# Kernel tuning notes

Measured on AMD Instinct MI355X. Metric: run time of the kernel, lower is better.

The kernel has to match this reference:

```python
import jax, jax.numpy as jnp
import numpy as np

B, S, L, D, H, F, V = 8, 1024, 12, 768, 12, 3072, 21128
TITLE_LEN, CONTENTS_LEN = 64, 960
DH = D // H
NEG_INF = -1e9


def setup_inputs() -> dict:
    key = jax.random.key(0)
    ks = jax.random.split(key, 14)
    p = lambda k, shape: (0.02 * jax.random.normal(k, shape)).astype(jnp.float32)
    return {
        "x": jax.random.randint(ks[0], (B, S), 0, V),
        "y": jax.random.randint(ks[1], (B, CONTENTS_LEN), 0, V),
        "word_emb": p(ks[2], (V, D)),
        "pos_emb": p(ks[3], (S, D)),
        "type_emb": p(ks[4], (2, D)),
        "emb_ln_g": jnp.ones((D,), jnp.float32),
        "emb_ln_b": jnp.zeros((D,), jnp.float32),
        "Wq": p(ks[5], (L, D, D)), "bq": jnp.zeros((L, D), jnp.float32),
        "Wk": p(ks[6], (L, D, D)), "bk": jnp.zeros((L, D), jnp.float32),
        "Wv": p(ks[7], (L, D, D)), "bv": jnp.zeros((L, D), jnp.float32),
        "Wo": p(ks[8], (L, D, D)), "bo": jnp.zeros((L, D), jnp.float32),
        "ln1_g": jnp.ones((L, D), jnp.float32), "ln1_b": jnp.zeros((L, D), jnp.float32),
        "W1": p(ks[9], (L, D, F)), "b1": jnp.zeros((L, F), jnp.float32),
        "W2": p(ks[10], (L, F, D)), "b2": jnp.zeros((L, D), jnp.float32),
        "ln2_g": jnp.ones((L, D), jnp.float32), "ln2_b": jnp.zeros((L, D), jnp.float32),
        "cls_W": p(ks[11], (D, V)), "cls_b": jnp.zeros((V,), jnp.float32),
    }


def _ln(x, g, b):
    m = x.mean(-1, keepdims=True)
    v = jnp.mean((x - m) ** 2, -1, keepdims=True)
    return (x - m) * jax.lax.rsqrt(v + 1e-12) * g + b


def _forward(x, y, word_emb, pos_emb, type_emb, emb_ln_g, emb_ln_b,
             Wq, bq, Wk, bk, Wv, bv, Wo, bo, ln1_g, ln1_b,
             W1, b1, W2, b2, ln2_g, ln2_b, cls_W, cls_b):
    # prefix-LM mask: causal (tril) except fully-visible title block [S,S]
    mask = jnp.tril(jnp.ones((S, S), jnp.float32))
    mask = mask.at[:TITLE_LEN, :TITLE_LEN].set(1.0)
    bias = (1.0 - mask) * NEG_INF  # additive attention bias

    h = word_emb[x] + pos_emb[None, :, :] + type_emb[0]  # [B,S,D]
    h = _ln(h, emb_ln_g, emb_ln_b)

    scale = 1.0 / np.sqrt(DH).astype(np.float32)

    def step(h, p):
        Wq_, bq_, Wk_, bk_, Wv_, bv_, Wo_, bo_, g1, bb1, W1_, bf1, W2_, bf2, g2, bb2 = p
        q = (h @ Wq_ + bq_).reshape(B, S, H, DH)
        k = (h @ Wk_ + bk_).reshape(B, S, H, DH)
        v = (h @ Wv_ + bv_).reshape(B, S, H, DH)
        scores = jnp.einsum('bqhd,bkhd->bhqk', q, k) * scale + bias  # [B,H,S,S]
        a = jax.nn.softmax(scores, axis=-1)
        ctx = jnp.einsum('bhqk,bkhd->bqhd', a, v).reshape(B, S, D)
        h = _ln(h + ctx @ Wo_ + bo_, g1, bb1)
        ffn = jax.nn.gelu(h @ W1_ + bf1, approximate=False) @ W2_ + bf2
        h = _ln(h + ffn, g2, bb2)
        return h, None

    h, _ = jax.lax.scan(step, h, (Wq, bq, Wk, bk, Wv, bv, Wo, bo,
                                  ln1_g, ln1_b, W1, b1, W2, b2, ln2_g, ln2_b))

    logits = h[:, -CONTENTS_LEN:, :] @ cls_W + cls_b  # [B,C,V]
    logp = jax.nn.log_softmax(logits, axis=-1)
    valid = (y != -100)
    yc = jnp.where(valid, y, 0)
    nll = -jnp.take_along_axis(logp, yc[..., None], axis=-1)[..., 0]
    return jnp.sum(nll * valid) / jnp.maximum(jnp.sum(valid), 1)


def reference(x, y, word_emb, pos_emb, type_emb, emb_ln_g, emb_ln_b,
              Wq, bq, Wk, bk, Wv, bv, Wo, bo, ln1_g, ln1_b,
              W1, b1, W2, b2, ln2_g, ln2_b, cls_W, cls_b):
    return _forward(x, y, word_emb, pos_emb, type_emb, emb_ln_g, emb_ln_b,
                    Wq, bq, Wk, bk, Wv, bv, Wo, bo, ln1_g, ln1_b,
                    W1, b1, W2, b2, ln2_g, ln2_b, cls_W, cls_b)
```

## Files before the change

kernel.cpp:

```cpp
#include <hip/hip_runtime.h>

#define BB 8
#define SS 1024
#define LL 12
#define DD 768
#define HH 12
#define FF 3072
#define VV 21128
#define DH 64
#define CLEN 960
#define NROWS (BB * CLEN)
#define TOKS (BB * SS)
#define NQKV 2304
#define QKW 1536

typedef __attribute__((ext_vector_type(8))) short bh8;
typedef __attribute__((ext_vector_type(4))) float f32x4;
typedef __attribute__((ext_vector_type(4))) unsigned short us4;

__device__ __forceinline__ float bf2f(unsigned short u) {
    union { unsigned int i; float f; } c; c.i = ((unsigned int)u) << 16; return c.f;
}
__device__ __forceinline__ unsigned short f2bf(float f) {
    union { float f; unsigned int i; } c; c.f = f;
    unsigned int r = c.i + 0x7fffu + ((c.i >> 16) & 1u);
    return (unsigned short)(r >> 16);
}

#define GLOAD16(gsrc, ldst)                                                              \
    __builtin_amdgcn_global_load_lds((const __attribute__((address_space(1))) unsigned int*)(gsrc), \
                                     (__attribute__((address_space(3))) unsigned int*)(ldst), 16, 0, 0)

__device__ __forceinline__ float bsum256(float v, float* red) {
#pragma unroll
    for (int o = 32; o; o >>= 1) v += __shfl_down(v, o);
    if ((threadIdx.x & 63) == 0) red[threadIdx.x >> 6] = v;
    __syncthreads();
    float r = red[0] + red[1] + red[2] + red[3];
    __syncthreads();
    return r;
}

__global__ void transpose_f32_bf16(const float* __restrict__ in, unsigned short* __restrict__ out,
                                   int R, int C) {
    __shared__ float tile[32][33];
    int c0 = blockIdx.x << 5, r0 = blockIdx.y << 5;
    int tx = threadIdx.x, ty = threadIdx.y;
    for (int i = ty; i < 32; i += 8) {
        int r = r0 + i, c = c0 + tx;
        if (r < R && c < C) tile[i][tx] = in[(size_t)r * C + c];
    }
    __syncthreads();
    for (int i = ty; i < 32; i += 8) {
        int oc = c0 + i, orr = r0 + tx;
        if (oc < C && orr < R) out[(size_t)oc * R + orr] = f2bf(tile[tx][i]);
    }
}

__global__ void transpose_layer(const float* __restrict__ Wq, const float* __restrict__ Wk,
                                const float* __restrict__ Wv, const float* __restrict__ Wo,
                                const float* __restrict__ W1, const float* __restrict__ W2,
                                unsigned short* __restrict__ wqkvT, unsigned short* __restrict__ woT,
                                unsigned short* __restrict__ w1T, unsigned short* __restrict__ w2T) {
    __shared__ float tile[32][33];
    int t = blockIdx.x;
    const float* src;
    unsigned short* dst;
    int R, C, txt, tt;
    if (t < 1728) {
        int which = t / 576; tt = t % 576;
        src = which == 0 ? Wq : (which == 1 ? Wk : Wv);
        dst = wqkvT + (size_t)which * DD * DD; R = DD; C = DD; txt = 24;
    } else if (t < 2304) {
        tt = t - 1728; src = Wo; dst = woT; R = DD; C = DD; txt = 24;
    } else if (t < 4608) {
        tt = t - 2304; src = W1; dst = w1T; R = DD; C = FF; txt = 96;
    } else {
        tt = t - 4608; src = W2; dst = w2T; R = FF; C = DD; txt = 24;
    }
    int c0 = (tt % txt) << 5, r0 = (tt / txt) << 5;
    int tx = threadIdx.x, ty = threadIdx.y;
    for (int i = ty; i < 32; i += 8) tile[i][tx] = src[(size_t)(r0 + i) * C + c0 + tx];
    __syncthreads();
    for (int i = ty; i < 32; i += 8) dst[(size_t)(c0 + i) * R + r0 + tx] = f2bf(tile[tx][i]);
}

__global__ void concat_bias_all(const float* __restrict__ bq, const float* __restrict__ bk,
                                const float* __restrict__ bv, float* __restrict__ out) {
    int i = blockIdx.x * 256 + threadIdx.x;
    if (i >= LL * NQKV) return;
    int l = i / NQKV, c = i % NQKV;
    float v = c < DD ? bq[(size_t)l * DD + c]
                     : (c < 2 * DD ? bk[(size_t)l * DD + c - DD] : bv[(size_t)l * DD + c - 2 * DD]);
    out[i] = v;
}

__global__ __launch_bounds__(256) void embed_ln(const int* __restrict__ x, const float* __restrict__ we,
                                                const float* __restrict__ pe, const float* __restrict__ te,
                                                const float* __restrict__ g, const float* __restrict__ be,
                                                unsigned short* __restrict__ hb) {
    int row = blockIdx.x;
    int s = row & (SS - 1);
    int tok = x[row];
    int tid = threadIdx.x;
    __shared__ float red[4];
    float v[3];
#pragma unroll
    for (int i = 0; i < 3; i++) {
        int c = tid + i * 256;
        v[i] = we[(size_t)tok * DD + c] + pe[(size_t)s * DD + c] + te[c];
    }
    float mean = bsum256(v[0] + v[1] + v[2], red) * (1.f / DD);
    float d0 = v[0] - mean, d1 = v[1] - mean, d2 = v[2] - mean;
    float var = bsum256(d0 * d0 + d1 * d1 + d2 * d2, red) * (1.f / DD);
    float inv = rsqrtf(var + 1e-12f);
    size_t base = (size_t)row * DD;
#pragma unroll
    for (int i = 0; i < 3; i++) {
        int c = tid + i * 256;
        hb[base + c] = f2bf((v[i] - mean) * inv * g[c] + be[c]);
    }
}

__global__ __launch_bounds__(256) void add_ln(const unsigned short* __restrict__ res,
                                              const unsigned short* __restrict__ t,
                                              const float* __restrict__ g, const float* __restrict__ be,
                                              unsigned short* __restrict__ outb) {
    int row = blockIdx.x;
    int tid = threadIdx.x;
    __shared__ float red[4];
    size_t base = (size_t)row * DD;
    float v[3];
#pragma unroll
    for (int i = 0; i < 3; i++) {
        int c = tid + i * 256;
        v[i] = bf2f(res[base + c]) + bf2f(t[base + c]);
    }
    float mean = bsum256(v[0] + v[1] + v[2], red) * (1.f / DD);
    float d0 = v[0] - mean, d1 = v[1] - mean, d2 = v[2] - mean;
    float var = bsum256(d0 * d0 + d1 * d1 + d2 * d2, red) * (1.f / DD);
    float inv = rsqrtf(var + 1e-12f);
#pragma unroll
    for (int i = 0; i < 3; i++) {
        int c = tid + i * 256;
        outb[base + c] = f2bf((v[i] - mean) * inv * g[c] + be[c]);
    }
}

template <int MODE>
__global__ __launch_bounds__(256) void gemm128(const unsigned short* __restrict__ A,
                                               const unsigned short* __restrict__ BT,
                                               const float* __restrict__ bias, void* __restrict__ Cp,
                                               int M, int N, int K, int ldc, int SM,
                                               unsigned short* __restrict__ vt_out,
                                               const int* __restrict__ yv,
                                               float* __restrict__ stS, float* __restrict__ stT) {
    __shared__ __align__(16) unsigned short As[2][128 * 32];
    __shared__ __align__(16) unsigned short Bs[2][128 * 32];
    const int tid = threadIdx.x;
    const int lane = tid & 63, w = tid >> 6;
    const int fr = lane & 15, fg = lane >> 4;
    const int wr = w >> 1, wc = w & 1;

    const int Nt = gridDim.x;
    const int flat = blockIdx.y * Nt + blockIdx.x;
    const int per8 = (Nt * gridDim.y) >> 3;
    const int virt = (flat & 7) * per8 + (flat >> 3);
    const int bandSz = SM * Nt;
    const int band = virt / bandSz, rem = virt - band * bandSz;
    const int nt = rem / SM;
    const int mt = band * SM + (rem - nt * SM);
    const int m0 = mt << 7, n0 = nt << 7;

    const int srow = lane >> 2;
    const int skcol = (lane & 3) << 3;

    int arow0 = m0 + (w * 2 + 0) * 16 + srow;
    int arow1 = m0 + (w * 2 + 1) * 16 + srow;
    int brow0 = n0 + (w * 2 + 0) * 16 + srow;
    int brow1 = n0 + (w * 2 + 1) * 16 + srow;
    if (brow0 >= N) brow0 = N - 1;
    if (brow1 >= N) brow1 = N - 1;
    const unsigned short* aptr0 = A + (size_t)arow0 * K + skcol;
    const unsigned short* aptr1 = A + (size_t)arow1 * K + skcol;
    const unsigned short* bptr0 = BT + (size_t)brow0 * K + skcol;
    const unsigned short* bptr1 = BT + (size_t)brow1 * K + skcol;

    auto stage = [&](int bf, int k0) {
        GLOAD16(aptr0 + k0, &As[bf][(w * 2 + 0) * 512]);
        GLOAD16(aptr1 + k0, &As[bf][(w * 2 + 1) * 512]);
        GLOAD16(bptr0 + k0, &Bs[bf][(w * 2 + 0) * 512]);
        GLOAD16(bptr1 + k0, &Bs[bf][(w * 2 + 1) * 512]);
    };

    f32x4 acc[4][4] = {};
    stage(0, 0);
    __syncthreads();
    int cur = 0;
    for (int k0 = 0; k0 < K; k0 += 32) {
        if (k0 + 32 < K) stage(cur ^ 1, k0 + 32);
        bh8 a[4], b[4];
#pragma unroll
        for (int mi = 0; mi < 4; mi++) a[mi] = *(const bh8*)&As[cur][(wr * 64 + mi * 16 + fr) * 32 + fg * 8];
#pragma unroll
        for (int ni = 0; ni < 4; ni++) b[ni] = *(const bh8*)&Bs[cur][(wc * 64 + ni * 16 + fr) * 32 + fg * 8];
        __builtin_amdgcn_s_setprio(1);
#pragma unroll
        for (int mi = 0; mi < 4; mi++)
#pragma unroll
            for (int ni = 0; ni < 4; ni++)
                acc[mi][ni] = __builtin_amdgcn_mfma_f32_16x16x32_bf16(a[mi], b[ni], acc[mi][ni], 0, 0, 0);
        __builtin_amdgcn_s_setprio(0);
        __syncthreads();
        cur ^= 1;
    }

    unsigned short* Cb = (unsigned short*)Cp;
#pragma unroll
    for (int mi = 0; mi < 4; mi++) {
        int rbase = m0 + wr * 64 + mi * 16 + fg * 4;
        if (MODE == 3) {
            float e[4] = {0.f, 0.f, 0.f, 0.f};
            int yr[4];
#pragma unroll
            for (int r = 0; r < 4; r++) yr[r] = yv[rbase + r];
#pragma unroll
            for (int ni = 0; ni < 4; ni++) {
                int col = n0 + wc * 64 + ni * 16 + fr;
                if (col < N) {
                    float bb = bias[col];
#pragma unroll
                    for (int r = 0; r < 4; r++) {
                        float v = acc[mi][ni][r] + bb;
                        e[r] += __expf(v);
                        if (col == yr[r]) stT[rbase + r] = v;
                    }
                }
            }
#pragma unroll
            for (int r = 0; r < 4; r++) {
#pragma unroll
                for (int off = 1; off < 16; off <<= 1) e[r] += __shfl_xor(e[r], off);
                if (fr == 0) atomicAdd(&stS[rbase + r], e[r]);
            }
        } else {
#pragma unroll
            for (int ni = 0; ni < 4; ni++) {
                int col = n0 + wc * 64 + ni * 16 + fr;
                if (MODE == 4) {
                    float bb = bias[col];
                    if (col < 2 * DD) {
#pragma unroll
                        for (int r = 0; r < 4; r++)
                            Cb[(size_t)(rbase + r) * QKW + col] = f2bf(acc[mi][ni][r] + bb);
                    } else {
                        int g = col - 2 * DD, h = g >> 6, d = g & 63;
                        int bi = rbase >> 10, s0 = rbase & 1023;
                        us4 val;
#pragma unroll
                        for (int r = 0; r < 4; r++) val[r] = f2bf(acc[mi][ni][r] + bb);
                        *(us4*)&vt_out[(((size_t)bi * HH + h) * DH + d) * SS + s0] = val;
                    }
                } else if (col < N) {
                    float bb = bias[col];
#pragma unroll
                    for (int r = 0; r < 4; r++) {
                        float v = acc[mi][ni][r] + bb;
                        if (MODE == 2) v = 0.5f * v * (1.0f + erff(v * 0.70710678118f));
                        Cb[(size_t)(rbase + r) * ldc + col] = f2bf(v);
                    }
                }
            }
        }
    }
}

__global__ __launch_bounds__(256) void flash_attn(const unsigned short* __restrict__ qkbuf,
                                                  const unsigned short* __restrict__ VT,
                                                  unsigned short* __restrict__ ctxb) {
    const int bx = blockIdx.x;
    const int h = blockIdx.y, b = blockIdx.z;
    const int tid = threadIdx.x;
    const int lane = tid & 63, w = tid >> 6;
    const int fr = lane & 15, fg = lane >> 4;
    __shared__ unsigned short Qs[64][68];
    __shared__ unsigned short Ks[64][68];
    __shared__ unsigned short Vt[64][68];
    __shared__ unsigned short Ps[4][16][68];

    const int srow = tid >> 2, sd0 = (tid & 3) << 4;
    const unsigned short* kbase = qkbuf + (size_t)(b * SS + srow) * QKW + DD + h * 64 + sd0;
    const unsigned short* vbase = VT + (((size_t)b * HH + h) * DH + srow) * SS + sd0;

    bh8 kr0, kr1, vr0, vr1;
    auto ld_reg = [&](int kt) {
        const unsigned short* ks = kbase + (size_t)(kt * 64) * QKW;
        kr0 = *(const bh8*)ks;
        kr1 = *(const bh8*)(ks + 8);
        const unsigned short* vs = vbase + kt * 64;
        vr0 = *(const bh8*)vs;
        vr1 = *(const bh8*)(vs + 8);
    };

    for (int half = 0; half < 2; half++) {
        const int qt = (half == 0) ? 15 - bx : bx;
        __syncthreads();
        {
            const unsigned short* src = qkbuf + (size_t)(b * SS + qt * 64 + srow) * QKW + h * 64 + sd0;
            *(bh8*)&Qs[srow][sd0] = *(const bh8*)src;
            *(bh8*)&Qs[srow][sd0 + 8] = *(const bh8*)(src + 8);
        }

        f32x4 o[4] = {};
        float m[4], l[4];
#pragma unroll
        for (int r = 0; r < 4; r++) { m[r] = -3e30f; l[r] = 0.f; }

        const int nkt = (qt == 0) ? 1 : qt + 1;
        ld_reg(0);
        for (int kt = 0; kt < nkt; kt++) {
            __syncthreads();
            *(bh8*)&Ks[srow][sd0] = kr0;
            *(bh8*)&Ks[srow][sd0 + 8] = kr1;
            *(bh8*)&Vt[srow][sd0] = vr0;
            *(bh8*)&Vt[srow][sd0 + 8] = vr1;
            if (kt + 1 < nkt) ld_reg(kt + 1);
            __syncthreads();

            f32x4 s[4] = {};
            bh8 a0 = *(const bh8*)&Qs[w * 16 + fr][fg * 8];
            bh8 a1 = *(const bh8*)&Qs[w * 16 + fr][32 + fg * 8];
            __builtin_amdgcn_s_setprio(1);
#pragma unroll
            for (int cf = 0; cf < 4; cf++) {
                bh8 b0 = *(const bh8*)&Ks[cf * 16 + fr][fg * 8];
                bh8 b1 = *(const bh8*)&Ks[cf * 16 + fr][32 + fg * 8];
                s[cf] = __builtin_amdgcn_mfma_f32_16x16x32_bf16(a0, b0, s[cf], 0, 0, 0);
                s[cf] = __builtin_amdgcn_mfma_f32_16x16x32_bf16(a1, b1, s[cf], 0, 0, 0);
            }
            __builtin_amdgcn_s_setprio(0);

            const bool diag = (qt > 0) && (kt == qt);
#pragma unroll
            for (int cf = 0; cf < 4; cf++) {
#pragma unroll
                for (int r = 0; r < 4; r++) {
                    float v = s[cf][r] * 0.125f;
                    if (diag) {
                        int key = cf * 16 + fr;
                        int qrow = w * 16 + fg * 4 + r;
                        if (key > qrow) v = -1e30f;
                    }
                    s[cf][r] = v;
                }
            }
            float sc[4], mn[4];
#pragma unroll
            for (int r = 0; r < 4; r++) {
                float v = fmaxf(fmaxf(s[0][r], s[1][r]), fmaxf(s[2][r], s[3][r]));
#pragma unroll
                for (int off = 1; off < 16; off <<= 1) v = fmaxf(v, __shfl_xor(v, off));
                mn[r] = fmaxf(m[r], v);
                sc[r] = __expf(m[r] - mn[r]);
                m[r] = mn[r];
            }
#pragma unroll
            for (int cf = 0; cf < 4; cf++) {
#pragma unroll
                for (int r = 0; r < 4; r++) s[cf][r] = __expf(s[cf][r] - mn[r]);
            }
#pragma unroll
            for (int r = 0; r < 4; r++) {
                float v = s[0][r] + s[1][r] + s[2][r] + s[3][r];
#pragma unroll
                for (int off = 1; off < 16; off <<= 1) v += __shfl_xor(v, off);
                l[r] = l[r] * sc[r] + v;
            }
#pragma unroll
            for (int df = 0; df < 4; df++) {
#pragma unroll
                for (int r = 0; r < 4; r++) o[df][r] *= sc[r];
            }
#pragma unroll
            for (int cf = 0; cf < 4; cf++) {
#pragma unroll
                for (int r = 0; r < 4; r++) Ps[w][fg * 4 + r][cf * 16 + fr] = f2bf(s[cf][r]);
            }
            bh8 pa0 = *(const bh8*)&Ps[w][fr][fg * 8];
            bh8 pa1 = *(const bh8*)&Ps[w][fr][32 + fg * 8];
            __builtin_amdgcn_s_setprio(1);
#pragma unroll
            for (int df = 0; df < 4; df++) {
                bh8 vb0 = *(const bh8*)&Vt[df * 16 + fr][fg * 8];
                bh8 vb1 = *(const bh8*)&Vt[df * 16 + fr][32 + fg * 8];
                o[df] = __builtin_amdgcn_mfma_f32_16x16x32_bf16(pa0, vb0, o[df], 0, 0, 0);
                o[df] = __builtin_amdgcn_mfma_f32_16x16x32_bf16(pa1, vb1, o[df], 0, 0, 0);
            }
            __builtin_amdgcn_s_setprio(0);
        }
#pragma unroll
        for (int df = 0; df < 4; df++) {
#pragma unroll
            for (int r = 0; r < 4; r++) {
                int q = qt * 64 + w * 16 + fg * 4 + r;
                float v = o[df][r] / l[r];
                ctxb[(((size_t)b * SS + q) * HH + h) * DH + df * 16 + fr] = f2bf(v);
            }
        }
    }
}

__global__ void gather_rows(const unsigned short* __restrict__ hb, unsigned short* __restrict__ hc) {
    int idx = blockIdx.x * 256 + threadIdx.x;
    if (idx >= NROWS * (DD / 8)) return;
    int g = idx / (DD / 8), c8 = (idx % (DD / 8)) * 8;
    int b = g / CLEN, cc = g % CLEN;
    *(bh8*)&hc[(size_t)g * DD + c8] = *(const bh8*)&hb[((size_t)(b * SS + 64 + cc)) * DD + c8];
}

__global__ void init_state(float* stS, float* stT) {
    int i = blockIdx.x * 256 + threadIdx.x;
    if (i < NROWS) { stS[i] = 0.f; stT[i] = 0.f; }
}

__global__ __launch_bounds__(256) void final_reduce(const float* __restrict__ stS,
                                                    const float* __restrict__ stT, const int* __restrict__ y,
                                                    float* __restrict__ out) {
    int tid = threadIdx.x;
    float s = 0.f, c = 0.f;
    for (int i = tid; i < NROWS; i += 256) {
        if (y[i] != -100) {
            s += logf(stS[i]) - stT[i];
            c += 1.f;
        }
    }
    __shared__ float red[4];
    float gs = bsum256(s, red);
    float gc = bsum256(c, red);
    if (tid == 0) out[0] = gs / fmaxf(gc, 1.f);
}

extern "C" void kernel_launch(void* const* d_in, const int* in_sizes, int n_in,
                              void* d_out, int out_size, void* d_ws, size_t ws_size,
                              hipStream_t stream) {
    const int* x = (const int*)d_in[0];
    const int* y = (const int*)d_in[1];
    const float* we = (const float*)d_in[2];
    const float* pe = (const float*)d_in[3];
    const float* te = (const float*)d_in[4];
    const float* eg = (const float*)d_in[5];
    const float* eb = (const float*)d_in[6];
    const float* Wq = (const float*)d_in[7];
    const float* bq = (const float*)d_in[8];
    const float* Wk = (const float*)d_in[9];
    const float* bk = (const float*)d_in[10];
    const float* Wv = (const float*)d_in[11];
    const float* bv = (const float*)d_in[12];
    const float* Wo = (const float*)d_in[13];
    const float* bo = (const float*)d_in[14];
    const float* g1 = (const float*)d_in[15];
    const float* b1n = (const float*)d_in[16];
    const float* W1 = (const float*)d_in[17];
    const float* b1 = (const float*)d_in[18];
    const float* W2 = (const float*)d_in[19];
    const float* b2 = (const float*)d_in[20];
    const float* g2 = (const float*)d_in[21];
    const float* b2n = (const float*)d_in[22];
    const float* clsW = (const float*)d_in[23];
    const float* clsb = (const float*)d_in[24];
    float* out = (float*)d_out;

    char* ws = (char*)d_ws;
    size_t off = 0;
    auto alloc = [&](size_t n) {
        void* p = ws + off;
        off += n;
        off = (off + 255) & ~(size_t)255;
        return p;
    };
    unsigned short* hb   = (unsigned short*)alloc((size_t)TOKS * DD * 2);
    unsigned short* h1b  = (unsigned short*)alloc((size_t)TOKS * DD * 2);
    unsigned short* tmpb = (unsigned short*)alloc((size_t)TOKS * DD * 2);
    unsigned short* qkbuf = (unsigned short*)alloc((size_t)TOKS * QKW * 2);
    unsigned short* vtb  = (unsigned short*)alloc((size_t)TOKS * DD * 2);
    unsigned short* ctxb = (unsigned short*)alloc((size_t)TOKS * DD * 2);
    unsigned short* ffnb = (unsigned short*)alloc((size_t)TOKS * FF * 2);
    unsigned short* wqkvT = (unsigned short*)alloc((size_t)NQKV * DD * 2);
    unsigned short* woT = (unsigned short*)alloc((size_t)DD * DD * 2);
    unsigned short* w1T = (unsigned short*)alloc((size_t)DD * FF * 2);
    unsigned short* w2T = (unsigned short*)alloc((size_t)DD * FF * 2);
    unsigned short* clsT = (unsigned short*)alloc((size_t)VV * DD * 2);
    unsigned short* hc = (unsigned short*)alloc((size_t)NROWS * DD * 2);
    float* bqkv = (float*)alloc((size_t)LL * NQKV * 4);
    float* stS = (float*)alloc(NROWS * 4);
    float* stT = (float*)alloc(NROWS * 4);

    dim3 tb(32, 8);
    transpose_f32_bf16<<<dim3((VV + 31) / 32, DD / 32), tb, 0, stream>>>(clsW, clsT, DD, VV);
    concat_bias_all<<<(LL * NQKV + 255) / 256, 256, 0, stream>>>(bq, bk, bv, bqkv);
    embed_ln<<<TOKS, 256, 0, stream>>>(x, we, pe, te, eg, eb, hb);

    for (int l = 0; l < LL; l++) {
        transpose_layer<<<6912, tb, 0, stream>>>(Wq + (size_t)l * DD * DD, Wk + (size_t)l * DD * DD,
                                                 Wv + (size_t)l * DD * DD, Wo + (size_t)l * DD * DD,
                                                 W1 + (size_t)l * DD * FF, W2 + (size_t)l * FF * DD,
                                                 wqkvT, woT, w1T, w2T);

        gemm128<4><<<dim3(NQKV / 128, TOKS / 128), 256, 0, stream>>>(hb, wqkvT, bqkv + (size_t)l * NQKV,
                                                                     qkbuf, TOKS, NQKV, DD, NQKV, 8, vtb,
                                                                     nullptr, nullptr, nullptr);

        flash_attn<<<dim3(8, HH, BB), 256, 0, stream>>>(qkbuf, vtb, ctxb);

        gemm128<1><<<dim3(DD / 128, TOKS / 128), 256, 0, stream>>>(ctxb, woT, bo + (size_t)l * DD, tmpb,
                                                                   TOKS, DD, DD, DD, 8, nullptr,
                                                                   nullptr, nullptr, nullptr);
        add_ln<<<TOKS, 256, 0, stream>>>(hb, tmpb, g1 + (size_t)l * DD, b1n + (size_t)l * DD, h1b);

        gemm128<2><<<dim3(FF / 128, TOKS / 128), 256, 0, stream>>>(h1b, w1T, b1 + (size_t)l * FF, ffnb,
                                                                   TOKS, FF, DD, FF, 8, nullptr,
                                                                   nullptr, nullptr, nullptr);
        gemm128<1><<<dim3(DD / 128, TOKS / 128), 256, 0, stream>>>(ffnb, w2T, b2 + (size_t)l * DD, tmpb,
                                                                   TOKS, DD, FF, DD, 8, nullptr,
                                                                   nullptr, nullptr, nullptr);
        add_ln<<<TOKS, 256, 0, stream>>>(h1b, tmpb, g2 + (size_t)l * DD, b2n + (size_t)l * DD, hb);
    }

    gather_rows<<<(NROWS * (DD / 8) + 255) / 256, 256, 0, stream>>>(hb, hc);
    init_state<<<(NROWS + 255) / 256, 256, 0, stream>>>(stS, stT);
    gemm128<3><<<dim3((VV + 127) / 128, NROWS / 128), 256, 0, stream>>>(hc, clsT, clsb, nullptr,
                                                                        NROWS, VV, DD, VV, 6, nullptr,
                                                                        y, stS, stT);
    final_reduce<<<1, 256, 0, stream>>>(stS, stT, y, out);
}
```

Baseline: 3.868 ms.

## Swizzle GEMM LDS layout, batch all-layer weight transposes, fuse state init

Applies an XOR swizzle to the k-column offset used for GEMM shared-memory staging and fragment reads, to reduce LDS bank conflicts. When the workspace is large enough, all layers' weights are transposed to bf16 in one launch rather than one launch per layer. The stS/stT zeroing is folded into gather_rows, which removes one small launch. The batched path needs much more workspace and falls back to per-layer transposes when it is not available.

```diff
diff --git a/kernel.cpp b/kernel.cpp
--- a/kernel.cpp
+++ b/kernel.cpp
@@ -55,6 +55,39 @@
         int oc = c0 + i, orr = r0 + tx;
         if (oc < C && orr < R) out[(size_t)oc * R + orr] = f2bf(tile[tx][i]);
     }
+}
+
+__global__ void transpose_all(const float* __restrict__ Wq, const float* __restrict__ Wk,
+                              const float* __restrict__ Wv, const float* __restrict__ Wo,
+                              const float* __restrict__ W1, const float* __restrict__ W2,
+                              unsigned short* __restrict__ wqkvT, unsigned short* __restrict__ woT,
+                              unsigned short* __restrict__ w1T, unsigned short* __restrict__ w2T) {
+    __shared__ float tile[32][33];
+    int t0 = blockIdx.x;
+    int l = t0 / 6912, t = t0 - l * 6912;
+    const float* src;
+    unsigned short* dst;
+    int R, C, txt, tt;
+    if (t < 1728) {
+        int which = t / 576; tt = t % 576;
+        src = (which == 0 ? Wq : (which == 1 ? Wk : Wv)) + (size_t)l * DD * DD;
+        dst = wqkvT + (size_t)l * NQKV * DD + (size_t)which * DD * DD;
+        R = DD; C = DD; txt = 24;
+    } else if (t < 2304) {
+        tt = t - 1728; src = Wo + (size_t)l * DD * DD; dst = woT + (size_t)l * DD * DD;
+        R = DD; C = DD; txt = 24;
+    } else if (t < 4608) {
+        tt = t - 2304; src = W1 + (size_t)l * DD * FF; dst = w1T + (size_t)l * DD * FF;
+        R = DD; C = FF; txt = 96;
+    } else {
+        tt = t - 4608; src = W2 + (size_t)l * FF * DD; dst = w2T + (size_t)l * FF * DD;
+        R = FF; C = DD; txt = 24;
+    }
+    int c0 = (tt % txt) << 5, r0 = (tt / txt) << 5;
+    int tx = threadIdx.x, ty = threadIdx.y;
+    for (int i = ty; i < 32; i += 8) tile[i][tx] = src[(size_t)(r0 + i) * C + c0 + tx];
+    __syncthreads();
+    for (int i = ty; i < 32; i += 8) dst[(size_t)(c0 + i) * R + r0 + tx] = f2bf(tile[tx][i]);
 }
 
 __global__ void transpose_layer(const float* __restrict__ Wq, const float* __restrict__ Wk,
@@ -173,7 +206,7 @@
     const int m0 = mt << 7, n0 = nt << 7;
 
     const int srow = lane >> 2;
-    const int skcol = (lane & 3) << 3;
+    const int skcol = (((lane & 3) ^ ((lane >> 3) & 3)) << 3);
 
     int arow0 = m0 + (w * 2 + 0) * 16 + srow;
     int arow1 = m0 + (w * 2 + 1) * 16 + srow;
@@ -193,6 +226,8 @@
         GLOAD16(bptr1 + k0, &Bs[bf][(w * 2 + 1) * 512]);
     };
 
+    const int rdcol = ((fg ^ ((fr >> 1) & 3)) << 3);
+
     f32x4 acc[4][4] = {};
     stage(0, 0);
     __syncthreads();
@@ -201,9 +236,9 @@
         if (k0 + 32 < K) stage(cur ^ 1, k0 + 32);
         bh8 a[4], b[4];
 #pragma unroll
-        for (int mi = 0; mi < 4; mi++) a[mi] = *(const bh8*)&As[cur][(wr * 64 + mi * 16 + fr) * 32 + fg * 8];
-#pragma unroll
-        for (int ni = 0; ni < 4; ni++) b[ni] = *(const bh8*)&Bs[cur][(wc * 64 + ni * 16 + fr) * 32 + fg * 8];
+        for (int mi = 0; mi < 4; mi++) a[mi] = *(const bh8*)&As[cur][(wr * 64 + mi * 16 + fr) * 32 + rdcol];
+#pragma unroll
+        for (int ni = 0; ni < 4; ni++) b[ni] = *(const bh8*)&Bs[cur][(wc * 64 + ni * 16 + fr) * 32 + rdcol];
         __builtin_amdgcn_s_setprio(1);
 #pragma unroll
         for (int mi = 0; mi < 4; mi++)
@@ -410,17 +445,14 @@
     }
 }
 
-__global__ void gather_rows(const unsigned short* __restrict__ hb, unsigned short* __restrict__ hc) {
+__global__ void gather_rows(const unsigned short* __restrict__ hb, unsigned short* __restrict__ hc,
+                            float* __restrict__ stS, float* __restrict__ stT) {
     int idx = blockIdx.x * 256 + threadIdx.x;
+    if (idx < NROWS) { stS[idx] = 0.f; stT[idx] = 0.f; }
     if (idx >= NROWS * (DD / 8)) return;
     int g = idx / (DD / 8), c8 = (idx % (DD / 8)) * 8;
     int b = g / CLEN, cc = g % CLEN;
     *(bh8*)&hc[(size_t)g * DD + c8] = *(const bh8*)&hb[((size_t)(b * SS + 64 + cc)) * DD + c8];
-}
-
-__global__ void init_state(float* stS, float* stT) {
-    int i = blockIdx.x * 256 + threadIdx.x;
-    if (i < NROWS) { stS[i] = 0.f; stT[i] = 0.f; }
 }
 
 __global__ __launch_bounds__(256) void final_reduce(const float* __restrict__ stS,
@@ -485,49 +517,56 @@
     unsigned short* vtb  = (unsigned short*)alloc((size_t)TOKS * DD * 2);
     unsigned short* ctxb = (unsigned short*)alloc((size_t)TOKS * DD * 2);
     unsigned short* ffnb = (unsigned short*)alloc((size_t)TOKS * FF * 2);
-    unsigned short* wqkvT = (unsigned short*)alloc((size_t)NQKV * DD * 2);
-    unsigned short* woT = (unsigned short*)alloc((size_t)DD * DD * 2);
-    unsigned short* w1T = (unsigned short*)alloc((size_t)DD * FF * 2);
-    unsigned short* w2T = (unsigned short*)alloc((size_t)DD * FF * 2);
     unsigned short* clsT = (unsigned short*)alloc((size_t)VV * DD * 2);
     unsigned short* hc = (unsigned short*)alloc((size_t)NROWS * DD * 2);
     float* bqkv = (float*)alloc((size_t)LL * NQKV * 4);
     float* stS = (float*)alloc(NROWS * 4);
     float* stT = (float*)alloc(NROWS * 4);
 
+    size_t needAll = off + ((size_t)LL * (NQKV + DD + FF + FF) * DD * 2) + 4096;
+    const bool bigWs = ws_size >= needAll;
+    const int WL = bigWs ? LL : 1;
+    unsigned short* wqkvT = (unsigned short*)alloc((size_t)WL * NQKV * DD * 2);
+    unsigned short* woT = (unsigned short*)alloc((size_t)WL * DD * DD * 2);
+    unsigned short* w1T = (unsigned short*)alloc((size_t)WL * DD * FF * 2);
+    unsigned short* w2T = (unsigned short*)alloc((size_t)WL * DD * FF * 2);
+
     dim3 tb(32, 8);
     transpose_f32_bf16<<<dim3((VV + 31) / 32, DD / 32), tb, 0, stream>>>(clsW, clsT, DD, VV);
     concat_bias_all<<<(LL * NQKV + 255) / 256, 256, 0, stream>>>(bq, bk, bv, bqkv);
+    if (bigWs)
+        transpose_all<<<LL * 6912, tb, 0, stream>>>(Wq, Wk, Wv, Wo, W1, W2, wqkvT, woT, w1T, w2T);
     embed_ln<<<TOKS, 256, 0, stream>>>(x, we, pe, te, eg, eb, hb);
 
     for (int l = 0; l < LL; l++) {
-        transpose_layer<<<6912, tb, 0, stream>>>(Wq + (size_t)l * DD * DD, Wk + (size_t)l * DD * DD,
-                                                 Wv + (size_t)l * DD * DD, Wo + (size_t)l * DD * DD,
-                                                 W1 + (size_t)l * DD * FF, W2 + (size_t)l * FF * DD,
-                                                 wqkvT, woT, w1T, w2T);
-
-        gemm128<4><<<dim3(NQKV / 128, TOKS / 128), 256, 0, stream>>>(hb, wqkvT, bqkv + (size_t)l * NQKV,
-                                                                     qkbuf, TOKS, NQKV, DD, NQKV, 8, vtb,
-                                                                     nullptr, nullptr, nullptr);
+        const int wl = bigWs ? l : 0;
+        if (!bigWs)
+            transpose_layer<<<6912, tb, 0, stream>>>(Wq + (size_t)l * DD * DD, Wk + (size_t)l * DD * DD,
+                                                     Wv + (size_t)l * DD * DD, Wo + (size_t)l * DD * DD,
+                                                     W1 + (size_t)l * DD * FF, W2 + (size_t)l * FF * DD,
+                                                     wqkvT, woT, w1T, w2T);
+
+        gemm128<4><<<dim3(NQKV / 128, TOKS / 128), 256, 0, stream>>>(
+            hb, wqkvT + (size_t)wl * NQKV * DD, bqkv + (size_t)l * NQKV,
+            qkbuf, TOKS, NQKV, DD, NQKV, 8, vtb, nullptr, nullptr, nullptr);
 
         flash_attn<<<dim3(8, HH, BB), 256, 0, stream>>>(qkbuf, vtb, ctxb);
 
-        gemm128<1><<<dim3(DD / 128, TOKS / 128), 256, 0, stream>>>(ctxb, woT, bo + (size_t)l * DD, tmpb,
-                                                                   TOKS, DD, DD, DD, 8, nullptr,
-                                                                   nullptr, nullptr, nullptr);
+        gemm128<1><<<dim3(DD / 128, TOKS / 128), 256, 0, stream>>>(
+            ctxb, woT + (size_t)wl * DD * DD, bo + (size_t)l * DD, tmpb,
+            TOKS, DD, DD, DD, 8, nullptr, nullptr, nullptr, nullptr);
         add_ln<<<TOKS, 256, 0, stream>>>(hb, tmpb, g1 + (size_t)l * DD, b1n + (size_t)l * DD, h1b);
 
-        gemm128<2><<<dim3(FF / 128, TOKS / 128), 256, 0, stream>>>(h1b, w1T, b1 + (size_t)l * FF, ffnb,
-                                                                   TOKS, FF, DD, FF, 8, nullptr,
-                                                                   nullptr, nullptr, nullptr);
-        gemm128<1><<<dim3(DD / 128, TOKS / 128), 256, 0, stream>>>(ffnb, w2T, b2 + (size_t)l * DD, tmpb,
-                                                                   TOKS, DD, FF, DD, 8, nullptr,
-                                                                   nullptr, nullptr, nullptr);
+        gemm128<2><<<dim3(FF / 128, TOKS / 128), 256, 0, stream>>>(
+            h1b, w1T + (size_t)wl * DD * FF, b1 + (size_t)l * FF, ffnb,
+            TOKS, FF, DD, FF, 8, nullptr, nullptr, nullptr, nullptr);
+        gemm128<1><<<dim3(DD / 128, TOKS / 128), 256, 0, stream>>>(
+            ffnb, w2T + (size_t)wl * DD * FF, b2 + (size_t)l * DD, tmpb,
+            TOKS, DD, FF, DD, 8, nullptr, nullptr, nullptr, nullptr);
         add_ln<<<TOKS, 256, 0, stream>>>(h1b, tmpb, g2 + (size_t)l * DD, b2n + (size_t)l * DD, hb);
     }
 
-    gather_rows<<<(NROWS * (DD / 8) + 255) / 256, 256, 0, stream>>>(hb, hc);
-    init_state<<<(NROWS + 255) / 256, 256, 0, stream>>>(stS, stT);
+    gather_rows<<<(NROWS * (DD / 8) + 255) / 256, 256, 0, stream>>>(hb, hc, stS, stT);
     gemm128<3><<<dim3((VV + 127) / 128, NROWS / 128), 256, 0, stream>>>(hc, clsT, clsb, nullptr,
                                                                         NROWS, VV, DD, VV, 6, nullptr,
                                                                         y, stS, stT);
```

Measured after the change: 4.213 ms. 8.9% more time.
